# Performance work log

Measured on AMD Instinct MI355X. Metric: run time of the kernel, lower is better.

Reference implementation:

```python
import jax, jax.numpy as jnp
import numpy as np

EMB, HEADS, T_BLK = 1024, 16, 2048
B, T = 2, 2048
HD = EMB // HEADS


def setup_inputs() -> dict:
    key = jax.random.key(0)
    ks = jax.random.split(key, 9)
    s = 1.0 / np.sqrt(EMB)
    return {
        "x": jax.random.normal(ks[0], (B, T, EMB), jnp.float32),
        "Wq": jax.random.normal(ks[1], (EMB, EMB), jnp.float32) * s,
        "bq": jax.random.normal(ks[2], (EMB,), jnp.float32) * s,
        "Wk": jax.random.normal(ks[3], (EMB, EMB), jnp.float32) * s,
        "bk": jax.random.normal(ks[4], (EMB,), jnp.float32) * s,
        "Wv": jax.random.normal(ks[5], (EMB, EMB), jnp.float32) * s,
        "bv": jax.random.normal(ks[6], (EMB,), jnp.float32) * s,
        "Wo": jax.random.normal(ks[7], (EMB, EMB), jnp.float32) * s,
        "bo": jax.random.normal(ks[8], (EMB,), jnp.float32) * s,
    }


def reference(x, Wq, bq, Wk, bk, Wv, bv, Wo, bo):
    # eval mode: dropout is identity
    Bn, Tn, C = x.shape
    def proj(W, b):
        y = x @ W.T + b                      # [B,T,C]
        return y.reshape(Bn, Tn, HEADS, HD).transpose(0, 2, 1, 3)  # [B,H,T,hd]
    q, k, v = proj(Wq, bq), proj(Wk, bk), proj(Wv, bv)
    scores = jnp.einsum('bhqd,bhkd->bhqk', q, k) * (HD ** -0.5)  # [B,H,T,T]
    causal = jnp.tril(jnp.ones((Tn, Tn), dtype=bool))
    scores = jnp.where(causal, scores, -jnp.inf)
    w = jax.nn.softmax(scores, axis=-1)
    out = jnp.einsum('bhqk,bhkd->bhqd', w, v)                    # [B,H,T,hd]
    out = out.transpose(0, 2, 1, 3).reshape(Bn, Tn, C)
    return out @ Wo.T + bo
```

## Files before the change

kernel.cpp:

```cpp
#include <hip/hip_runtime.h>
#include <stdint.h>

#define EMB   1024
#define HEADS 16
#define HD    64
#define BB    2
#define TT    2048
#define MTOT  (BB*TT)
#define LDP   72

#define ELX (4194304u)
#define ELW (1048576u)

#define CSCALE (0.125f * 1.44269504088896f)

typedef __attribute__((ext_vector_type(8))) short short8;
typedef __attribute__((ext_vector_type(4))) float f32x4;
typedef __attribute__((ext_vector_type(4))) unsigned short us4;

__device__ __forceinline__ float bf2f(ushort u) {
  union { uint32_t u; float f; } x; x.u = ((uint32_t)u) << 16; return x.f;
}
__device__ __forceinline__ ushort f2bf(float f) {
  union { float f; uint32_t u; } x; x.f = f;
  uint32_t u = x.u;
  u += 0x7fffu + ((u >> 16) & 1u);
  return (ushort)(u >> 16);
}
__device__ __forceinline__ uint32_t pack2(uint32_t lo, uint32_t hi) {
  return (lo >> 16) | (hi & 0xFFFF0000u);
}
__device__ __forceinline__ short8 pack8(f32x4 a, f32x4 b) {
  union { f32x4 v; uint32_t u[4]; } A, B;
  A.v = a; B.v = b;
  union { uint32_t d[4]; short8 s; } R;
  R.d[0] = pack2(A.u[0], A.u[1]);
  R.d[1] = pack2(A.u[2], A.u[3]);
  R.d[2] = pack2(B.u[0], B.u[1]);
  R.d[3] = pack2(B.u[2], B.u[3]);
  return R.s;
}
__device__ __forceinline__ short8 cvt8_rne(const float* f) {
  f32x4 a = *(const f32x4*)f;
  f32x4 b = *(const f32x4*)(f + 4);
  short8 r;
  r[0] = (short)f2bf(a[0]); r[1] = (short)f2bf(a[1]);
  r[2] = (short)f2bf(a[2]); r[3] = (short)f2bf(a[3]);
  r[4] = (short)f2bf(b[0]); r[5] = (short)f2bf(b[1]);
  r[6] = (short)f2bf(b[2]); r[7] = (short)f2bf(b[3]);
  return r;
}

__device__ __forceinline__ void gll16(const void* g, void* l) {
  __builtin_amdgcn_global_load_lds((const __attribute__((address_space(1))) void*)g,
                                   (__attribute__((address_space(3))) void*)l,
                                   16, 0, 0);
}

__global__ void detect_dtype(const uint32_t* __restrict__ x, int* __restrict__ flag) {
  const int lane = threadIdx.x & 63;
  int cnt = 0;
#pragma unroll
  for (int i = 0; i < 4; ++i) {
    const uint32_t v = x[lane * 4 + i];
    const uint32_t e = ((v & 0xFFFFu) >> 7) & 0xFFu;
    cnt += (e >= 0x70u && e <= 0x8Fu) ? 1 : 0;
  }
#pragma unroll
  for (int off = 1; off < 64; off <<= 1) cnt += __shfl_xor(cnt, off);
  if (lane == 0) *flag = (cnt > 128) ? 1 : 0;
}

__global__ __launch_bounds__(256) void convert4(const void* __restrict__ w0,
                                                const void* __restrict__ w1,
                                                const void* __restrict__ w2,
                                                const void* __restrict__ x,
                                                ushort* __restrict__ w3,
                                                ushort* __restrict__ xb,
                                                const int* __restrict__ flag) {
  const size_t i = ((size_t)blockIdx.x * 256 + threadIdx.x) * 8;
  const int isbf = *flag;
  if (i < 3u * ELW) {
    const int wi = (int)(i >> 20);
    const size_t off = i & (ELW - 1);
    const void* src = (wi == 0) ? w0 : (wi == 1) ? w1 : w2;
    if (isbf) *(short8*)(w3 + i) = *(const short8*)((const ushort*)src + off);
    else      *(short8*)(w3 + i) = cvt8_rne((const float*)src + off);
  } else {
    const size_t j = i - 3u * ELW;
    if (isbf) *(short8*)(xb + j) = *(const short8*)((const ushort*)x + j);
    else      *(short8*)(xb + j) = cvt8_rne((const float*)x + j);
  }
}

#define ASZ (256 * 64)
#define BSZ (192 * 64)

__device__ __forceinline__ void qkv_core(const ushort* __restrict__ xb,
                                         const ushort* __restrict__ W,
                                         int m0, int n0r,
                                         ushort* As0, ushort* Bs0,
                                         f32x4 acc[8][3]) {
  const int tid  = threadIdx.x;
  const int w    = tid >> 6;
  const int lane = tid & 63;
  const int quad = lane >> 4;
  const int l16  = lane & 15;
  const int wr   = w >> 2, wc = w & 3;

  const int prow = tid >> 3;
  const int c    = tid & 7;
  const int sw   = c ^ (prow & 7);
  const int rsw  = l16 & 7;

  auto stageB = [&](int cur, int kt) {
#pragma unroll
    for (int g = 0; g < 3; ++g)
      gll16(W + (size_t)(n0r + g * 64 + prow) * EMB + kt * 64 + sw * 8,
            Bs0 + cur * BSZ + g * 4096 + w * 512);
  };
  auto stageA = [&](int cur, int kt) {
#pragma unroll
    for (int g = 0; g < 4; ++g)
      gll16(xb + (size_t)(m0 + g * 64 + prow) * EMB + kt * 64 + sw * 8,
            As0 + cur * ASZ + g * 4096 + w * 512);
  };

  stageB(0, 0);
  stageA(0, 0);
  __syncthreads();

  for (int t = 0; t < 16; ++t) {
    const int cur = t & 1, nxt = cur ^ 1;
    if (t < 15) {
      stageB(nxt, t + 1);
      stageA(nxt, t + 1);
    }

    const ushort* Ab = As0 + cur * ASZ;
    const ushort* Bb = Bs0 + cur * BSZ;
    short8 bf_[3][2];
#pragma unroll
    for (int ni = 0; ni < 3; ++ni)
#pragma unroll
      for (int ks = 0; ks < 2; ++ks)
        bf_[ni][ks] = *(const short8*)&Bb[(wc * 48 + ni * 16 + l16) * 64 +
                                          ((ks * 4 + quad) ^ rsw) * 8];
#pragma unroll
    for (int mi = 0; mi < 8; ++mi) {
      const int arow = (wr * 128 + mi * 16 + l16) * 64;
      short8 a0 = *(const short8*)&Ab[arow + ((quad) ^ rsw) * 8];
      short8 a1 = *(const short8*)&Ab[arow + ((4 + quad) ^ rsw) * 8];
#pragma unroll
      for (int ni = 0; ni < 3; ++ni) {
        acc[mi][ni] = __builtin_amdgcn_mfma_f32_16x16x32_bf16(a0, bf_[ni][0], acc[mi][ni], 0, 0, 0);
        acc[mi][ni] = __builtin_amdgcn_mfma_f32_16x16x32_bf16(a1, bf_[ni][1], acc[mi][ni], 0, 0, 0);
      }
    }
    __syncthreads();
  }
}

__global__ __launch_bounds__(512, 2) void qkv_pipe(const ushort* __restrict__ xb,
                                                   const ushort* __restrict__ w3,
                                                   const void* __restrict__ bq,
                                                   const void* __restrict__ bk,
                                                   const void* __restrict__ bv,
                                                   ushort* __restrict__ qo,
                                                   ushort* __restrict__ ko,
                                                   ushort* __restrict__ vo,
                                                   const int* __restrict__ flag) {
  __shared__ __align__(16) ushort As2[2 * ASZ];
  __shared__ __align__(16) ushort Bs2[2 * BSZ];
  const int bid = blockIdx.x;
  const int xcd = bid & 7;
  const int mt  = xcd * 2 + ((bid >> 3) & 1);
  const int nt  = bid >> 4;
  const int m0  = mt * 256;
  const int n0r = nt * 192;

  f32x4 acc[8][3];
#pragma unroll
  for (int a = 0; a < 8; ++a)
#pragma unroll
    for (int b = 0; b < 3; ++b) acc[a][b] = (f32x4){0.f, 0.f, 0.f, 0.f};

  qkv_core(xb, w3, m0, n0r, As2, Bs2, acc);

  const int isbf = *flag;
  const int tid  = threadIdx.x;
  const int w    = tid >> 6;
  const int lane = tid & 63;
  const int quad = lane >> 4;
  const int l16  = lane & 15;
  const int wr   = w >> 2, wc = w & 3;

#pragma unroll
  for (int ni = 0; ni < 3; ++ni) {
    const int n   = n0r + wc * 48 + ni * 16 + l16;
    const int mat = n >> 10, nn = n & 1023;
    const void* bias = (mat == 0) ? bq : (mat == 1) ? bk : bv;
    const float bv_ = isbf ? bf2f(((const ushort*)bias)[nn]) : ((const float*)bias)[nn];
    const int h = nn >> 6, d = nn & 63;
    const float sc = (mat == 0) ? CSCALE : 1.0f;
    ushort* dqk = (mat == 0) ? qo : ko;
#pragma unroll
    for (int mi = 0; mi < 8; ++mi) {
      const int m = m0 + wr * 128 + mi * 16 + quad * 4;
      const int b = m >> 11, tt = m & (TT - 1);
      if (mat == 2) {
        us4 pk;
#pragma unroll
        for (int r = 0; r < 4; ++r) pk[r] = f2bf(acc[mi][ni][r] + bv_);
        *(us4*)&vo[((size_t)((b * HEADS + h) * HD + d)) * TT + tt] = pk;
      } else {
#pragma unroll
        for (int r = 0; r < 4; ++r)
          dqk[((size_t)((b * HEADS + h) * TT + tt + r)) * HD + d] =
              f2bf((acc[mi][ni][r] + bv_) * sc);
      }
    }
  }
}

__global__ __launch_bounds__(256) void attn3(const ushort* __restrict__ qw,
                                             const ushort* __restrict__ kw,
                                             const ushort* __restrict__ vtw,
                                             ushort* __restrict__ out) {
  __shared__ __align__(16) ushort Ks[64 * 64];
  __shared__ __align__(16) ushort Vts[64 * 64];
  __shared__ __align__(16) ushort Ps[4][16 * 64];

  const int bid = blockIdx.x;
  const int j  = bid >> 8;
  const int r8 = bid & 255;
  const int qh = r8 & 31;
  const int bh = j * 8 + (r8 >> 5);
  int qt;
  if      (j == 0) qt = qh;
  else if (j == 1) qt = 31 - qh;
  else if (j == 2) qt = (qh + 16) & 31;
  else             qt = 31 - ((qh + 16) & 31);
  const int h = bh & (HEADS - 1);
  const int b = bh >> 4;

  const int tid  = threadIdx.x;
  const int w    = tid >> 6;
  const int lane = tid & 63;
  const int quad = lane >> 4;
  const int l16  = lane & 15;
  const int rsw  = l16 & 7;

  const size_t hoff = ((size_t)(b * HEADS + h)) * TT * HD;
  const ushort* Qg = qw + hoff;
  const ushort* Kg = kw + hoff;
  const ushort* Vg = vtw + hoff;
  const int q0 = qt * 64;

  short8 qf[2];
  {
    const ushort* qrow = Qg + (size_t)(q0 + w * 16 + l16) * HD;
    qf[0] = *(const short8*)(qrow + quad * 8);
    qf[1] = *(const short8*)(qrow + 32 + quad * 8);
  }

  const int row = tid >> 2;
  const int cq  = (tid & 3) * 2;
  const int s0  = (cq)     ^ (row & 7);
  const int s1  = (cq + 1) ^ (row & 7);
  const int c0  = cq * 8;
  const ushort* Kbase = Kg + (size_t)row * HD + c0;
  const ushort* Vbase = Vg + (size_t)row * TT + c0;

  float lsp[4] = {0.f, 0.f, 0.f, 0.f};
  f32x4 O[4];
#pragma unroll
  for (int ni = 0; ni < 4; ++ni) O[ni] = (f32x4){0.f, 0.f, 0.f, 0.f};

  auto compute_tile = [&](int kt) {
    f32x4 s[4];
#pragma unroll
    for (int ni = 0; ni < 4; ++ni) s[ni] = (f32x4){0.f, 0.f, 0.f, 0.f};
#pragma unroll
    for (int ks = 0; ks < 2; ++ks) {
#pragma unroll
      for (int ni = 0; ni < 4; ++ni) {
        short8 kb = *(const short8*)&Ks[(ni * 16 + l16) * 64 +
                                        ((ks * 4 + quad) ^ rsw) * 8];
        s[ni] = __builtin_amdgcn_mfma_f32_16x16x32_bf16(kb, qf[ks], s[ni], 0, 0, 0);
      }
    }
    if (kt == qt) {
      const int qq = w * 16 + l16;
#pragma unroll
      for (int ni = 0; ni < 4; ++ni) {
#pragma unroll
        for (int r = 0; r < 4; ++r)
          if (ni * 16 + quad * 4 + r > qq) s[ni][r] = -__builtin_inff();
      }
    }
#pragma unroll
    for (int ni = 0; ni < 4; ++ni) {
      union { float f; uint32_t u; } p0, p1, p2, p3;
      p0.f = exp2f(s[ni][0]); p1.f = exp2f(s[ni][1]);
      p2.f = exp2f(s[ni][2]); p3.f = exp2f(s[ni][3]);
      lsp[ni] += (p0.f + p1.f) + (p2.f + p3.f);
      uint2 dw;
      dw.x = pack2(p0.u, p1.u);
      dw.y = pack2(p2.u, p3.u);
      const int slot = (2 * ni + (quad >> 1)) ^ rsw;
      *(uint2*)&Ps[w][l16 * 64 + slot * 8 + (quad & 1) * 4] = dw;
    }
#pragma unroll
    for (int ks = 0; ks < 2; ++ks) {
      short8 a = *(const short8*)&Ps[w][l16 * 64 + ((ks * 4 + quad) ^ rsw) * 8];
#pragma unroll
      for (int ni = 0; ni < 4; ++ni) {
        short8 vb = *(const short8*)&Vts[(ni * 16 + l16) * 64 +
                                         ((ks * 4 + quad) ^ rsw) * 8];
        O[ni] = __builtin_amdgcn_mfma_f32_16x16x32_bf16(a, vb, O[ni], 0, 0, 0);
      }
    }
  };

  short8 ak0, ak1, av0, av1;
  short8 bk0, bk1, bv0, bv1;
  ak0 = *(const short8*)(Kbase);
  ak1 = *(const short8*)(Kbase + 8);
  av0 = *(const short8*)(Vbase);
  av1 = *(const short8*)(Vbase + 8);

  for (int kt = 0; kt <= qt; ) {
    __syncthreads();
    *(short8*)&Ks[row * 64 + s0 * 8]  = ak0;
    *(short8*)&Ks[row * 64 + s1 * 8]  = ak1;
    *(short8*)&Vts[row * 64 + s0 * 8] = av0;
    *(short8*)&Vts[row * 64 + s1 * 8] = av1;
    if (kt + 1 <= qt) {
      const size_t ko_ = (size_t)(kt + 1) * 64 * HD;
      bk0 = *(const short8*)(Kbase + ko_);
      bk1 = *(const short8*)(Kbase + ko_ + 8);
      bv0 = *(const short8*)(Vbase + (kt + 1) * 64);
      bv1 = *(const short8*)(Vbase + (kt + 1) * 64 + 8);
    }
    __syncthreads();
    compute_tile(kt);
    ++kt;
    if (kt > qt) break;

    __syncthreads();
    *(short8*)&Ks[row * 64 + s0 * 8]  = bk0;
    *(short8*)&Ks[row * 64 + s1 * 8]  = bk1;
    *(short8*)&Vts[row * 64 + s0 * 8] = bv0;
    *(short8*)&Vts[row * 64 + s1 * 8] = bv1;
    if (kt + 1 <= qt) {
      const size_t ko_ = (size_t)(kt + 1) * 64 * HD;
      ak0 = *(const short8*)(Kbase + ko_);
      ak1 = *(const short8*)(Kbase + ko_ + 8);
      av0 = *(const short8*)(Vbase + (kt + 1) * 64);
      av1 = *(const short8*)(Vbase + (kt + 1) * 64 + 8);
    }
    __syncthreads();
    compute_tile(kt);
    ++kt;
  }

  float lst = (lsp[0] + lsp[1]) + (lsp[2] + lsp[3]);
  lst += __shfl_xor(lst, 16);
  lst += __shfl_xor(lst, 32);

#pragma unroll
  for (int r = 0; r < 4; ++r) {
    const float inv = 1.0f / __shfl(lst, (lane & 48) | (quad * 4 + r));
    const int t = q0 + w * 16 + quad * 4 + r;
#pragma unroll
    for (int ni = 0; ni < 4; ++ni) {
      out[((size_t)(b * TT + t)) * EMB + h * HD + ni * 16 + l16] = f2bf(O[ni][r] * inv);
    }
  }
}

template<bool WBF>
__device__ __forceinline__ void proj_core(const ushort* __restrict__ A,
                                          const void* __restrict__ Wo,
                                          int m0, int n0,
                                          ushort* As, ushort* Ws,
                                          f32x4 acc[2][4]) {
  const int tid  = threadIdx.x;
  const int w    = tid >> 6;
  const int lane = tid & 63;
  const int quad = lane >> 4;
  const int l16  = lane & 15;
  const int arow = tid >> 1;
  const int acol = (tid & 1) * 32;
  const int brow = tid >> 2;
  const int bcol = (tid & 3) * 16;

  const size_t aoff = (size_t)(m0 + arow) * EMB + acol;
  const size_t boff = (size_t)(n0 + brow) * EMB + bcol;

  short8 ab[3][4];
  short8 wb[3][2];
  f32x4  wf[3][4];

#pragma unroll
  for (int s = 0; s < 2; ++s) {
#pragma unroll
    for (int i = 0; i < 4; ++i)
      ab[s][i] = *(const short8*)(A + aoff + 64 * s + 8 * i);
    if constexpr (WBF) {
      wb[s][0] = *(const short8*)((const ushort*)Wo + boff + 64 * s);
      wb[s][1] = *(const short8*)((const ushort*)Wo + boff + 64 * s + 8);
    } else {
#pragma unroll
      for (int i = 0; i < 4; ++i)
        wf[s][i] = *(const f32x4*)((const float*)Wo + boff + 64 * s + 4 * i);
    }
  }

#pragma unroll
  for (int it = 0; it < 16; ++it) {
    const int k0 = it * 64;
    const int cur = it % 3, nxt = (it + 2) % 3;
    __syncthreads();
#pragma unroll
    for (int i = 0; i < 4; ++i)
      *(short8*)&As[arow * LDP + acol + 8 * i] = ab[cur][i];
    if constexpr (WBF) {
      *(short8*)&Ws[brow * LDP + bcol]     = wb[cur][0];
      *(short8*)&Ws[brow * LDP + bcol + 8] = wb[cur][1];
    } else {
      *(short8*)&Ws[brow * LDP + bcol]     = pack8(wf[cur][0], wf[cur][1]);
      *(short8*)&Ws[brow * LDP + bcol + 8] = pack8(wf[cur][2], wf[cur][3]);
    }
    if (it + 2 < 16) {
      const int kn = k0 + 128;
#pragma unroll
      for (int i = 0; i < 4; ++i)
        ab[nxt][i] = *(const short8*)(A + aoff + kn + 8 * i);
      if constexpr (WBF) {
        wb[nxt][0] = *(const short8*)((const ushort*)Wo + boff + kn);
        wb[nxt][1] = *(const short8*)((const ushort*)Wo + boff + kn + 8);
      } else {
#pragma unroll
        for (int i = 0; i < 4; ++i)
          wf[nxt][i] = *(const f32x4*)((const float*)Wo + boff + kn + 4 * i);
      }
    }
    __syncthreads();

#pragma unroll
    for (int ks = 0; ks < 2; ++ks) {
      short8 a_[2], b_[4];
#pragma unroll
      for (int i = 0; i < 2; ++i)
        a_[i] = *(const short8*)&As[(w * 32 + i * 16 + l16) * LDP + ks * 32 + quad * 8];
#pragma unroll
      for (int i = 0; i < 4; ++i)
        b_[i] = *(const short8*)&Ws[(i * 16 + l16) * LDP + ks * 32 + quad * 8];
#pragma unroll
      for (int mi = 0; mi < 2; ++mi)
#pragma unroll
        for (int ni = 0; ni < 4; ++ni)
          acc[mi][ni] = __builtin_amdgcn_mfma_f32_16x16x32_bf16(a_[mi], b_[ni], acc[mi][ni], 0, 0, 0);
    }
  }
}

__global__ __launch_bounds__(256) void proj_pipe(const ushort* __restrict__ A,
                                                 const void* __restrict__ Wo,
                                                 const void* __restrict__ bo,
                                                 void* __restrict__ out,
                                                 const int* __restrict__ flag) {
  __shared__ __align__(16) ushort As[128 * LDP];
  __shared__ __align__(16) ushort Ws[64 * LDP];
  const int nt = blockIdx.x & 15;
  const int mt = blockIdx.x >> 4;
  const int n0 = nt * 64;
  const int m0 = mt * 128;

  f32x4 acc[2][4];
#pragma unroll
  for (int i = 0; i < 2; ++i)
#pragma unroll
    for (int jj = 0; jj < 4; ++jj) acc[i][jj] = (f32x4){0.f, 0.f, 0.f, 0.f};

  const int isbf = *flag;
  if (isbf) proj_core<true >(A, Wo, m0, n0, As, Ws, acc);
  else      proj_core<false>(A, Wo, m0, n0, As, Ws, acc);

  const int tid  = threadIdx.x;
  const int w    = tid >> 6;
  const int lane = tid & 63;
  const int quad = lane >> 4;
  const int l16  = lane & 15;

#pragma unroll
  for (int ni = 0; ni < 4; ++ni) {
    const int n = n0 + ni * 16 + l16;
    const float bv_ = isbf ? bf2f(((const ushort*)bo)[n]) : ((const float*)bo)[n];
#pragma unroll
    for (int mi = 0; mi < 2; ++mi) {
#pragma unroll
      for (int r = 0; r < 4; ++r) {
        const int m = m0 + w * 32 + mi * 16 + quad * 4 + r;
        const float v = acc[mi][ni][r] + bv_;
        if (isbf) ((ushort*)out)[(size_t)m * EMB + n] = f2bf(v);
        else      ((float*) out)[(size_t)m * EMB + n] = v;
      }
    }
  }
}

extern "C" void kernel_launch(void* const* d_in, const int* in_sizes, int n_in,
                              void* d_out, int out_size, void* d_ws, size_t ws_size,
                              hipStream_t stream) {
  const void* x  = d_in[0];
  const void* Wq = d_in[1];
  const void* bq = d_in[2];
  const void* Wk = d_in[3];
  const void* bk = d_in[4];
  const void* Wv = d_in[5];
  const void* bv = d_in[6];
  const void* Wo = d_in[7];
  const void* bo = d_in[8];

  int* flag = (int*)d_ws;
  ushort* base = (ushort*)((char*)d_ws + 256);

  ushort* q_ws  = base;
  ushort* k_ws  = q_ws + ELX;
  ushort* vt_ws = k_ws + ELX;
  ushort* w3    = vt_ws + ELX;
  ushort* o_ws  = vt_ws + ELX;
  ushort* xb    = (ushort*)d_out;

  detect_dtype<<<dim3(1), dim3(64), 0, stream>>>((const uint32_t*)x, flag);
  convert4<<<dim3(3584), dim3(256), 0, stream>>>(Wq, Wk, Wv, x, w3, xb, flag);
  qkv_pipe<<<dim3(256), dim3(512), 0, stream>>>(xb, w3, bq, bk, bv,
                                                q_ws, k_ws, vt_ws, flag);
  attn3<<<dim3(1024), dim3(256), 0, stream>>>(q_ws, k_ws, vt_ws, o_ws);
  proj_pipe<<<dim3(512), dim3(256), 0, stream>>>(o_ws, Wo, bo, d_out, flag);
}
```

Measured before the change: 199.9 us.

## Double-buffer K/V tiles in LDS using direct global-to-LDS loads in attention

Replaces the register-staged K/V prefetch (global→register→LDS with two barriers per tile) with double-buffered LDS tiles filled by direct global-to-LDS loads (gll16), issued one tile ahead of compute. This cuts register pressure and one barrier per iteration, letting loads for the next tile overlap the MFMA work on the current one. In exchange it doubles K/V LDS usage, which may lower occupancy, and it depends on the gll16 helper and its swizzled address mapping being correct.

```diff
diff --git a/kernel.cpp b/kernel.cpp
--- a/kernel.cpp
+++ b/kernel.cpp
@@ -227,8 +227,8 @@
                                              const ushort* __restrict__ kw,
                                              const ushort* __restrict__ vtw,
                                              ushort* __restrict__ out) {
-  __shared__ __align__(16) ushort Ks[64 * 64];
-  __shared__ __align__(16) ushort Vts[64 * 64];
+  __shared__ __align__(16) ushort Ks[2][64 * 64];
+  __shared__ __align__(16) ushort Vts[2][64 * 64];
   __shared__ __align__(16) ushort Ps[4][16 * 64];
 
   const int bid = blockIdx.x;
@@ -264,20 +264,25 @@
     qf[1] = *(const short8*)(qrow + 32 + quad * 8);
   }
 
-  const int row = tid >> 2;
-  const int cq  = (tid & 3) * 2;
-  const int s0  = (cq)     ^ (row & 7);
-  const int s1  = (cq + 1) ^ (row & 7);
-  const int c0  = cq * 8;
-  const ushort* Kbase = Kg + (size_t)row * HD + c0;
-  const ushort* Vbase = Vg + (size_t)row * TT + c0;
+  const int prow = tid >> 3;
+  const int sc_  = (tid & 7) ^ (prow & 7);
+  const ushort* Kb = Kg + (size_t)prow * HD + sc_ * 8;
+  const ushort* Vb = Vg + (size_t)prow * TT + sc_ * 8;
+
+  auto stage = [&](int buf, int kt) {
+#pragma unroll
+    for (int g = 0; g < 2; ++g) {
+      gll16(Kb + (size_t)(kt * 64 + g * 32) * HD, &Ks[buf][g * 2048 + w * 512]);
+      gll16(Vb + (size_t)(g * 32) * TT + kt * 64, &Vts[buf][g * 2048 + w * 512]);
+    }
+  };
 
   float lsp[4] = {0.f, 0.f, 0.f, 0.f};
   f32x4 O[4];
 #pragma unroll
   for (int ni = 0; ni < 4; ++ni) O[ni] = (f32x4){0.f, 0.f, 0.f, 0.f};
 
-  auto compute_tile = [&](int kt) {
+  auto compute_tile = [&](int kt, int cur) {
     f32x4 s[4];
 #pragma unroll
     for (int ni = 0; ni < 4; ++ni) s[ni] = (f32x4){0.f, 0.f, 0.f, 0.f};
@@ -285,8 +290,8 @@
     for (int ks = 0; ks < 2; ++ks) {
 #pragma unroll
       for (int ni = 0; ni < 4; ++ni) {
-        short8 kb = *(const short8*)&Ks[(ni * 16 + l16) * 64 +
-                                        ((ks * 4 + quad) ^ rsw) * 8];
+        short8 kb = *(const short8*)&Ks[cur][(ni * 16 + l16) * 64 +
+                                            ((ks * 4 + quad) ^ rsw) * 8];
         s[ni] = __builtin_amdgcn_mfma_f32_16x16x32_bf16(kb, qf[ks], s[ni], 0, 0, 0);
       }
     }
@@ -316,53 +321,20 @@
       short8 a = *(const short8*)&Ps[w][l16 * 64 + ((ks * 4 + quad) ^ rsw) * 8];
 #pragma unroll
       for (int ni = 0; ni < 4; ++ni) {
-        short8 vb = *(const short8*)&Vts[(ni * 16 + l16) * 64 +
-                                         ((ks * 4 + quad) ^ rsw) * 8];
+        short8 vb = *(const short8*)&Vts[cur][(ni * 16 + l16) * 64 +
+                                              ((ks * 4 + quad) ^ rsw) * 8];
         O[ni] = __builtin_amdgcn_mfma_f32_16x16x32_bf16(a, vb, O[ni], 0, 0, 0);
       }
     }
   };
 
-  short8 ak0, ak1, av0, av1;
-  short8 bk0, bk1, bv0, bv1;
-  ak0 = *(const short8*)(Kbase);
-  ak1 = *(const short8*)(Kbase + 8);
-  av0 = *(const short8*)(Vbase);
-  av1 = *(const short8*)(Vbase + 8);
-
-  for (int kt = 0; kt <= qt; ) {
+  stage(0, 0);
+  __syncthreads();
+  for (int kt = 0; kt <= qt; ++kt) {
+    const int cur = kt & 1;
+    if (kt < qt) stage(cur ^ 1, kt + 1);
+    compute_tile(kt, cur);
     __syncthreads();
-    *(short8*)&Ks[row * 64 + s0 * 8]  = ak0;
-    *(short8*)&Ks[row * 64 + s1 * 8]  = ak1;
-    *(short8*)&Vts[row * 64 + s0 * 8] = av0;
-    *(short8*)&Vts[row * 64 + s1 * 8] = av1;
-    if (kt + 1 <= qt) {
-      const size_t ko_ = (size_t)(kt + 1) * 64 * HD;
-      bk0 = *(const short8*)(Kbase + ko_);
-      bk1 = *(const short8*)(Kbase + ko_ + 8);
-      bv0 = *(const short8*)(Vbase + (kt + 1) * 64);
-      bv1 = *(const short8*)(Vbase + (kt + 1) * 64 + 8);
-    }
-    __syncthreads();
-    compute_tile(kt);
-    ++kt;
-    if (kt > qt) break;
-
-    __syncthreads();
-    *(short8*)&Ks[row * 64 + s0 * 8]  = bk0;
-    *(short8*)&Ks[row * 64 + s1 * 8]  = bk1;
-    *(short8*)&Vts[row * 64 + s0 * 8] = bv0;
-    *(short8*)&Vts[row * 64 + s1 * 8] = bv1;
-    if (kt + 1 <= qt) {
-      const size_t ko_ = (size_t)(kt + 1) * 64 * HD;
-      ak0 = *(const short8*)(Kbase + ko_);
-      ak1 = *(const short8*)(Kbase + ko_ + 8);
-      av0 = *(const short8*)(Vbase + (kt + 1) * 64);
-      av1 = *(const short8*)(Vbase + (kt + 1) * 64 + 8);
-    }
-    __syncthreads();
-    compute_tile(kt);
-    ++kt;
   }
 
   float lst = (lsp[0] + lsp[1]) + (lsp[2] + lsp[3]);
```

After: 212.7 us. 1.06x slower.

## Rewrite output projection with async LDS loads, bigger tiles and pre-converted Wo

Applied to the files above, without the earlier changes.

Wo is converted to bf16 in a separate kernel into the now-free q workspace. The output projection then uses 128x128 tiles with 512 threads and double-buffered global_load_lds staging into an XOR-swizzled LDS layout. The register-staged triple-buffer with padded LDS is removed. Blocks are mapped so the m-tiles are spread across XCDs for L2 reuse. This cuts register traffic and fp32 weight loads, at the cost of an extra kernel launch and fewer blocks in flight.

```diff
diff --git a/kernel.cpp b/kernel.cpp
--- a/kernel.cpp
+++ b/kernel.cpp
@@ -7,7 +7,6 @@
 #define BB    2
 #define TT    2048
 #define MTOT  (BB*TT)
-#define LDP   72
 
 #define ELX (4194304u)
 #define ELW (1048576u)
@@ -29,16 +28,6 @@
 }
 __device__ __forceinline__ uint32_t pack2(uint32_t lo, uint32_t hi) {
   return (lo >> 16) | (hi & 0xFFFF0000u);
-}
-__device__ __forceinline__ short8 pack8(f32x4 a, f32x4 b) {
-  union { f32x4 v; uint32_t u[4]; } A, B;
-  A.v = a; B.v = b;
-  union { uint32_t d[4]; short8 s; } R;
-  R.d[0] = pack2(A.u[0], A.u[1]);
-  R.d[1] = pack2(A.u[2], A.u[3]);
-  R.d[2] = pack2(B.u[0], B.u[1]);
-  R.d[3] = pack2(B.u[2], B.u[3]);
-  return R.s;
 }
 __device__ __forceinline__ short8 cvt8_rne(const float* f) {
   f32x4 a = *(const f32x4*)f;
@@ -93,6 +82,14 @@
   }
 }
 
+__global__ __launch_bounds__(256) void convertW1(const void* __restrict__ wo,
+                                                 ushort* __restrict__ dst,
+                                                 const int* __restrict__ flag) {
+  const size_t i = ((size_t)blockIdx.x * 256 + threadIdx.x) * 8;
+  if (*flag) *(short8*)(dst + i) = *(const short8*)((const ushort*)wo + i);
+  else       *(short8*)(dst + i) = cvt8_rne((const float*)wo + i);
+}
+
 #define ASZ (256 * 64)
 #define BSZ (192 * 64)
 
@@ -380,130 +377,95 @@
   }
 }
 
-template<bool WBF>
-__device__ __forceinline__ void proj_core(const ushort* __restrict__ A,
-                                          const void* __restrict__ Wo,
-                                          int m0, int n0,
-                                          ushort* As, ushort* Ws,
-                                          f32x4 acc[2][4]) {
+#define PASZ (128 * 64)
+
+__global__ __launch_bounds__(512, 2) void proj_pipe(const ushort* __restrict__ A,
+                                                    const ushort* __restrict__ Wb,
+                                                    const void* __restrict__ bo,
+                                                    void* __restrict__ out,
+                                                    const int* __restrict__ flag) {
+  __shared__ __align__(16) ushort As2[2 * PASZ];
+  __shared__ __align__(16) ushort Bs2[2 * PASZ];
+  const int bid = blockIdx.x;
+  const int xcd = bid & 7;
+  const int mt  = xcd * 4 + ((bid >> 3) & 3);
+  const int nt  = bid >> 5;
+  const int m0  = mt * 128;
+  const int n0  = nt * 128;
+
   const int tid  = threadIdx.x;
   const int w    = tid >> 6;
   const int lane = tid & 63;
   const int quad = lane >> 4;
   const int l16  = lane & 15;
-  const int arow = tid >> 1;
-  const int acol = (tid & 1) * 32;
-  const int brow = tid >> 2;
-  const int bcol = (tid & 3) * 16;
-
-  const size_t aoff = (size_t)(m0 + arow) * EMB + acol;
-  const size_t boff = (size_t)(n0 + brow) * EMB + bcol;
-
-  short8 ab[3][4];
-  short8 wb[3][2];
-  f32x4  wf[3][4];
-
-#pragma unroll
-  for (int s = 0; s < 2; ++s) {
-#pragma unroll
-    for (int i = 0; i < 4; ++i)
-      ab[s][i] = *(const short8*)(A + aoff + 64 * s + 8 * i);
-    if constexpr (WBF) {
-      wb[s][0] = *(const short8*)((const ushort*)Wo + boff + 64 * s);
-      wb[s][1] = *(const short8*)((const ushort*)Wo + boff + 64 * s + 8);
-    } else {
-#pragma unroll
-      for (int i = 0; i < 4; ++i)
-        wf[s][i] = *(const f32x4*)((const float*)Wo + boff + 64 * s + 4 * i);
-    }
-  }
-
-#pragma unroll
-  for (int it = 0; it < 16; ++it) {
-    const int k0 = it * 64;
-    const int cur = it % 3, nxt = (it + 2) % 3;
+  const int wr   = w >> 2, wc = w & 3;
+
+  const int prow = tid >> 3;
+  const int sw   = (tid & 7) ^ (prow & 7);
+  const int rsw  = l16 & 7;
+
+  f32x4 acc[4][2];
+#pragma unroll
+  for (int i = 0; i < 4; ++i)
+#pragma unroll
+    for (int jj = 0; jj < 2; ++jj) acc[i][jj] = (f32x4){0.f, 0.f, 0.f, 0.f};
+
+  auto stageA = [&](int cur, int kt) {
+#pragma unroll
+    for (int g = 0; g < 2; ++g)
+      gll16(A + (size_t)(m0 + g * 64 + prow) * EMB + kt * 64 + sw * 8,
+            As2 + cur * PASZ + g * 4096 + w * 512);
+  };
+  auto stageB = [&](int cur, int kt) {
+#pragma unroll
+    for (int g = 0; g < 2; ++g)
+      gll16(Wb + (size_t)(n0 + g * 64 + prow) * EMB + kt * 64 + sw * 8,
+            Bs2 + cur * PASZ + g * 4096 + w * 512);
+  };
+
+  stageA(0, 0);
+  stageB(0, 0);
+  __syncthreads();
+
+  for (int t = 0; t < 16; ++t) {
+    const int cur = t & 1, nxt = cur ^ 1;
+    if (t < 15) {
+      stageA(nxt, t + 1);
+      stageB(nxt, t + 1);
+    }
+    const ushort* Ab = As2 + cur * PASZ;
+    const ushort* Bb = Bs2 + cur * PASZ;
+    short8 bf_[2][2];
+#pragma unroll
+    for (int ni = 0; ni < 2; ++ni)
+#pragma unroll
+      for (int ks = 0; ks < 2; ++ks)
+        bf_[ni][ks] = *(const short8*)&Bb[(wc * 32 + ni * 16 + l16) * 64 +
+                                          ((ks * 4 + quad) ^ rsw) * 8];
+#pragma unroll
+    for (int mi = 0; mi < 4; ++mi) {
+      const int arow = (wr * 64 + mi * 16 + l16) * 64;
+      short8 a0 = *(const short8*)&Ab[arow + ((quad) ^ rsw) * 8];
+      short8 a1 = *(const short8*)&Ab[arow + ((4 + quad) ^ rsw) * 8];
+#pragma unroll
+      for (int ni = 0; ni < 2; ++ni) {
+        acc[mi][ni] = __builtin_amdgcn_mfma_f32_16x16x32_bf16(a0, bf_[ni][0], acc[mi][ni], 0, 0, 0);
+        acc[mi][ni] = __builtin_amdgcn_mfma_f32_16x16x32_bf16(a1, bf_[ni][1], acc[mi][ni], 0, 0, 0);
+      }
+    }
     __syncthreads();
-#pragma unroll
-    for (int i = 0; i < 4; ++i)
-      *(short8*)&As[arow * LDP + acol + 8 * i] = ab[cur][i];
-    if constexpr (WBF) {
-      *(short8*)&Ws[brow * LDP + bcol]     = wb[cur][0];
-      *(short8*)&Ws[brow * LDP + bcol + 8] = wb[cur][1];
-    } else {
-      *(short8*)&Ws[brow * LDP + bcol]     = pack8(wf[cur][0], wf[cur][1]);
-      *(short8*)&Ws[brow * LDP + bcol + 8] = pack8(wf[cur][2], wf[cur][3]);
-    }
-    if (it + 2 < 16) {
-      const int kn = k0 + 128;
-#pragma unroll
-      for (int i = 0; i < 4; ++i)
-        ab[nxt][i] = *(const short8*)(A + aoff + kn + 8 * i);
-      if constexpr (WBF) {
-        wb[nxt][0] = *(const short8*)((const ushort*)Wo + boff + kn);
-        wb[nxt][1] = *(const short8*)((const ushort*)Wo + boff + kn + 8);
-      } else {
-#pragma unroll
-        for (int i = 0; i < 4; ++i)
-          wf[nxt][i] = *(const f32x4*)((const float*)Wo + boff + kn + 4 * i);
-      }
-    }
-    __syncthreads();
-
-#pragma unroll
-    for (int ks = 0; ks < 2; ++ks) {
-      short8 a_[2], b_[4];
-#pragma unroll
-      for (int i = 0; i < 2; ++i)
-        a_[i] = *(const short8*)&As[(w * 32 + i * 16 + l16) * LDP + ks * 32 + quad * 8];
-#pragma unroll
-      for (int i = 0; i < 4; ++i)
-        b_[i] = *(const short8*)&Ws[(i * 16 + l16) * LDP + ks * 32 + quad * 8];
-#pragma unroll
-      for (int mi = 0; mi < 2; ++mi)
-#pragma unroll
-        for (int ni = 0; ni < 4; ++ni)
-          acc[mi][ni] = __builtin_amdgcn_mfma_f32_16x16x32_bf16(a_[mi], b_[ni], acc[mi][ni], 0, 0, 0);
-    }
-  }
-}
-
-__global__ __launch_bounds__(256) void proj_pipe(const ushort* __restrict__ A,
-                                                 const void* __restrict__ Wo,
-                                                 const void* __restrict__ bo,
-                                                 void* __restrict__ out,
-                                                 const int* __restrict__ flag) {
-  __shared__ __align__(16) ushort As[128 * LDP];
-  __shared__ __align__(16) ushort Ws[64 * LDP];
-  const int nt = blockIdx.x & 15;
-  const int mt = blockIdx.x >> 4;
-  const int n0 = nt * 64;
-  const int m0 = mt * 128;
-
-  f32x4 acc[2][4];
-#pragma unroll
-  for (int i = 0; i < 2; ++i)
-#pragma unroll
-    for (int jj = 0; jj < 4; ++jj) acc[i][jj] = (f32x4){0.f, 0.f, 0.f, 0.f};
+  }
 
   const int isbf = *flag;
-  if (isbf) proj_core<true >(A, Wo, m0, n0, As, Ws, acc);
-  else      proj_core<false>(A, Wo, m0, n0, As, Ws, acc);
-
-  const int tid  = threadIdx.x;
-  const int w    = tid >> 6;
-  const int lane = tid & 63;
-  const int quad = lane >> 4;
-  const int l16  = lane & 15;
-
-#pragma unroll
-  for (int ni = 0; ni < 4; ++ni) {
-    const int n = n0 + ni * 16 + l16;
+#pragma unroll
+  for (int ni = 0; ni < 2; ++ni) {
+    const int n = n0 + wc * 32 + ni * 16 + l16;
     const float bv_ = isbf ? bf2f(((const ushort*)bo)[n]) : ((const float*)bo)[n];
 #pragma unroll
-    for (int mi = 0; mi < 2; ++mi) {
+    for (int mi = 0; mi < 4; ++mi) {
 #pragma unroll
       for (int r = 0; r < 4; ++r) {
-        const int m = m0 + w * 32 + mi * 16 + quad * 4 + r;
+        const int m = m0 + wr * 64 + mi * 16 + quad * 4 + r;
         const float v = acc[mi][ni][r] + bv_;
         if (isbf) ((ushort*)out)[(size_t)m * EMB + n] = f2bf(v);
         else      ((float*) out)[(size_t)m * EMB + n] = v;
@@ -534,11 +496,13 @@
   ushort* w3    = vt_ws + ELX;
   ushort* o_ws  = vt_ws + ELX;
   ushort* xb    = (ushort*)d_out;
+  ushort* wo_b  = q_ws;
 
   detect_dtype<<<dim3(1), dim3(64), 0, stream>>>((const uint32_t*)x, flag);
   convert4<<<dim3(3584), dim3(256), 0, stream>>>(Wq, Wk, Wv, x, w3, xb, flag);
   qkv_pipe<<<dim3(256), dim3(512), 0, stream>>>(xb, w3, bq, bk, bv,
                                                 q_ws, k_ws, vt_ws, flag);
   attn3<<<dim3(1024), dim3(256), 0, stream>>>(q_ws, k_ws, vt_ws, o_ws);
-  proj_pipe<<<dim3(512), dim3(256), 0, stream>>>(o_ws, Wo, bo, d_out, flag);
-}
+  convertW1<<<dim3(512), dim3(256), 0, stream>>>(Wo, wo_b, flag);
+  proj_pipe<<<dim3(256), dim3(512), 0, stream>>>(o_ws, wo_b, bo, d_out, flag);
+}
```

New measurement: 198.5 us. No clear change (-0.7%).
